# Optimization experiments

Hardware: AMD Instinct MI355X
Metric: run time of the kernel (lower is better)

Reference implementation:

```python
import jax, jax.numpy as jnp
import numpy as np

B, S, L, H = 8, 4, 512, 768
N_SPANS, T_MAX = 4096, 16
N_PAIRS = 16384


def setup_inputs() -> dict:
    key = jax.random.key(0)
    k1, k2, k3, k4, k5, k6 = jax.random.split(key, 6)
    hidden = jax.random.normal(k1, (B, S, L, H), dtype=jnp.float32)
    span_doc = jax.random.randint(k2, (N_SPANS,), 0, B, dtype=jnp.int32)
    # per-span padded, sorted subtoken indices into the flattened S*L window axis
    span_tok = jnp.sort(jax.random.randint(k3, (N_SPANS, T_MAX), 0, S * L, dtype=jnp.int32), axis=1)
    span_len = jax.random.randint(k4, (N_SPANS,), 1, T_MAX + 1, dtype=jnp.int32)
    pair_i = jax.random.randint(k5, (N_PAIRS,), 0, N_SPANS, dtype=jnp.int32)
    pair_j = jax.random.randint(k6, (N_PAIRS,), 0, N_SPANS, dtype=jnp.int32)
    return {"hidden": hidden, "span_doc": span_doc, "span_tok": span_tok,
            "span_len": span_len, "pair_i": pair_i, "pair_j": pair_j}


def reference(hidden, span_doc, span_tok, span_len, pair_i, pair_j):
    # hidden: [B, S, L, H]; flatten windows so span_tok indexes S*L directly
    b, s, l, h = hidden.shape
    hf = hidden.reshape(b, s * l, h)
    # ragged gather: [N, T, H]
    g = hf[span_doc[:, None], span_tok]
    n, t = span_tok.shape
    mask = (jnp.arange(t, dtype=jnp.int32)[None, :] < span_len[:, None])  # [N, T]
    denom = span_len.astype(hidden.dtype)[:, None]
    mean = jnp.sum(g * mask[..., None].astype(hidden.dtype), axis=1) / denom  # [N, H]
    first = g[:, 0]                                      # first subtoken of span
    last = g[jnp.arange(n), span_len - 1]                # last valid subtoken
    reprs = jnp.concatenate([first, mean, last], axis=-1)  # [N, 3H]
    pairs = jnp.concatenate([reprs[pair_i], reprs[pair_j]], axis=-1)  # [P, 6H]
    return pairs
```

## Files before the change

### kernel.cpp

```cpp
#include <hip/hip_runtime.h>


#define SPAN_HF4  192
#define SPAN_TMAX 16
#define SPAN_SL   2048
#define REPR_F4   576
#define OUT_F4    1152
#define MAX_SPANS 4096

typedef float f4nt __attribute__((ext_vector_type(4)));

__device__ __forceinline__ void nt_store_f4(const float4 v, float4* p) {
    f4nt t;
    t.x = v.x; t.y = v.y; t.z = v.z; t.w = v.w;
    __builtin_nontemporal_store(t, reinterpret_cast<f4nt*>(p));
}

__device__ __forceinline__ void store_repr(float4* o, int c,
                                           const float4 a0, const float4 a1,
                                           const float4 a2) {
    nt_store_f4(a0, &o[c]);
    nt_store_f4(a1, &o[SPAN_HF4 + c]);
    nt_store_f4(a2, &o[2 * SPAN_HF4 + c]);
}


__global__ void zero_counts_kernel(int* __restrict__ counts, int n) {
    const int i = blockIdx.x * blockDim.x + threadIdx.x;
    if (i < n) counts[i] = 0;
}

__global__ void count_uses_kernel(const int* __restrict__ pair_i,
                                  const int* __restrict__ pair_j,
                                  int* __restrict__ counts, int n_pairs) {
    const int p = blockIdx.x * blockDim.x + threadIdx.x;
    if (p < n_pairs) {
        atomicAdd(&counts[pair_i[p]], 1);
        atomicAdd(&counts[pair_j[p]], 1);
    }
}

__global__ __launch_bounds__(1024)
void scan_offsets_kernel(const int* __restrict__ counts,
                         int* __restrict__ offsets,
                         int* __restrict__ cursor,
                         int n_spans) {
    __shared__ int sums[1024];
    const int t = threadIdx.x;
    const int base = t * 4;
    int c0 = 0, c1 = 0, c2 = 0, c3 = 0;
    if (base     < n_spans) c0 = counts[base];
    if (base + 1 < n_spans) c1 = counts[base + 1];
    if (base + 2 < n_spans) c2 = counts[base + 2];
    if (base + 3 < n_spans) c3 = counts[base + 3];
    sums[t] = c0 + c1 + c2 + c3;
    __syncthreads();
    for (int off = 1; off < 1024; off <<= 1) {
        const int v = (t >= off) ? sums[t - off] : 0;
        __syncthreads();
        sums[t] += v;
        __syncthreads();
    }
    const int excl = (t == 0) ? 0 : sums[t - 1];
    const int o0 = excl, o1 = o0 + c0, o2 = o1 + c1, o3 = o2 + c2;
    if (base     < n_spans) { offsets[base]     = o0; cursor[base]     = o0; }
    if (base + 1 < n_spans) { offsets[base + 1] = o1; cursor[base + 1] = o1; }
    if (base + 2 < n_spans) { offsets[base + 2] = o2; cursor[base + 2] = o2; }
    if (base + 3 < n_spans) { offsets[base + 3] = o3; cursor[base + 3] = o3; }
    if (t == 1023) offsets[n_spans] = sums[1023];
}

__global__ void fill_targets_kernel(const int* __restrict__ pair_i,
                                    const int* __restrict__ pair_j,
                                    int* __restrict__ cursor,
                                    int* __restrict__ targets,
                                    int n_pairs) {
    const int p = blockIdx.x * blockDim.x + threadIdx.x;
    if (p < n_pairs) {
        const int a = atomicAdd(&cursor[pair_i[p]], 1);
        targets[a] = p * 2;
        const int b = atomicAdd(&cursor[pair_j[p]], 1);
        targets[b] = p * 2 + 1;
    }
}


__global__ __launch_bounds__(192)
void span_scatter_kernel(
    const float4* __restrict__ hidden,
    const int*    __restrict__ span_doc,
    const int*    __restrict__ span_tok,
    const int*    __restrict__ span_len,
    const int*    __restrict__ offsets,
    const int*    __restrict__ targets,
    float4*       __restrict__ out,
    int n_spans)
{
    const int c = threadIdx.x;
    const int s = blockIdx.x;
    if (s >= n_spans) return;

    const int doc   = __builtin_amdgcn_readfirstlane(span_doc[s]);
    const int len   = __builtin_amdgcn_readfirstlane(span_len[s]);
    const int start = __builtin_amdgcn_readfirstlane(offsets[s]);
    const int end   = __builtin_amdgcn_readfirstlane(offsets[s + 1]);
    const int* toks = span_tok + s * SPAN_TMAX;
    const float4* base = hidden + (size_t)doc * (SPAN_SL * SPAN_HF4);

    float4 first, last;
    float sx, sy, sz, sw;
    {
        const float4 v = base[(size_t)toks[0] * SPAN_HF4 + c];
        first = v; last = v;
        sx = v.x; sy = v.y; sz = v.z; sw = v.w;
    }
    #pragma unroll
    for (int t = 1; t < SPAN_TMAX; ++t) {
        const int tc = (t < len) ? t : (len - 1);
        const float4 v = base[(size_t)toks[tc] * SPAN_HF4 + c];
        last = v;
        const float m = (t < len) ? 1.f : 0.f;
        sx += v.x * m; sy += v.y * m; sz += v.z * m; sw += v.w * m;
    }
    const float inv = 1.0f / (float)len;
    const float4 a1 = make_float4(sx * inv, sy * inv, sz * inv, sw * inv);

    int k = start;
    for (; k + 4 <= end; k += 4) {
        const int t0 = __builtin_amdgcn_readfirstlane(targets[k]);
        const int t1 = __builtin_amdgcn_readfirstlane(targets[k + 1]);
        const int t2 = __builtin_amdgcn_readfirstlane(targets[k + 2]);
        const int t3 = __builtin_amdgcn_readfirstlane(targets[k + 3]);
        store_repr(out + (size_t)(t0 >> 1) * OUT_F4 + (size_t)(t0 & 1) * REPR_F4,
                   c, first, a1, last);
        store_repr(out + (size_t)(t1 >> 1) * OUT_F4 + (size_t)(t1 & 1) * REPR_F4,
                   c, first, a1, last);
        store_repr(out + (size_t)(t2 >> 1) * OUT_F4 + (size_t)(t2 & 1) * REPR_F4,
                   c, first, a1, last);
        store_repr(out + (size_t)(t3 >> 1) * OUT_F4 + (size_t)(t3 & 1) * REPR_F4,
                   c, first, a1, last);
    }
    for (; k < end; ++k) {
        const int tv = __builtin_amdgcn_readfirstlane(targets[k]);
        store_repr(out + (size_t)(tv >> 1) * OUT_F4 + (size_t)(tv & 1) * REPR_F4,
                   c, first, a1, last);
    }
}


__global__ __launch_bounds__(192)
void span_fused_kernel(
    const float4* __restrict__ hidden,
    const int*    __restrict__ span_doc,
    const int*    __restrict__ span_tok,
    const int*    __restrict__ span_len,
    const int*    __restrict__ pair_i,
    const int*    __restrict__ pair_j,
    float4*       __restrict__ out)
{
    const int p = blockIdx.x;
    const int c = threadIdx.x;
    const int si = pair_i[p];
    const int sj = pair_j[p];
    float4* orow = out + (size_t)p * OUT_F4;

    #pragma unroll
    for (int side = 0; side < 2; ++side) {
        const int s   = side ? sj : si;
        const int doc = span_doc[s];
        const int len = span_len[s];
        const int* toks = span_tok + s * SPAN_TMAX;
        const float4* base = hidden + (size_t)doc * (SPAN_SL * SPAN_HF4);

        float4 first = make_float4(0.f, 0.f, 0.f, 0.f);
        float4 last  = make_float4(0.f, 0.f, 0.f, 0.f);
        float sx = 0.f, sy = 0.f, sz = 0.f, sw = 0.f;
        #pragma unroll
        for (int t = 0; t < SPAN_TMAX; ++t) {
            const int tc = (t < len) ? t : (len - 1);
            const float4 v = base[(size_t)toks[tc] * SPAN_HF4 + c];
            if (t == 0) first = v;
            last = v;
            const float m = (t < len) ? 1.f : 0.f;
            sx += v.x * m; sy += v.y * m; sz += v.z * m; sw += v.w * m;
        }
        const float inv = 1.0f / (float)len;
        float4* o = orow + side * REPR_F4;
        nt_store_f4(first, &o[c]);
        nt_store_f4(make_float4(sx * inv, sy * inv, sz * inv, sw * inv),
                    &o[SPAN_HF4 + c]);
        nt_store_f4(last, &o[2 * SPAN_HF4 + c]);
    }
}


extern "C" void kernel_launch(void* const* d_in, const int* in_sizes, int n_in,
                              void* d_out, int out_size, void* d_ws, size_t ws_size,
                              hipStream_t stream) {
    const float4* hidden  = (const float4*)d_in[0];
    const int* span_doc   = (const int*)d_in[1];
    const int* span_tok   = (const int*)d_in[2];
    const int* span_len   = (const int*)d_in[3];
    const int* pair_i     = (const int*)d_in[4];
    const int* pair_j     = (const int*)d_in[5];
    float4* out           = (float4*)d_out;

    const int n_spans = in_sizes[1];
    const int n_pairs = in_sizes[4];

    auto align16 = [](size_t x) { return (x + 15) & ~(size_t)15; };
    const size_t counts_b  = align16((size_t)n_spans * sizeof(int));
    const size_t offsets_b = align16((size_t)(n_spans + 1) * sizeof(int));
    const size_t cursor_b  = align16((size_t)n_spans * sizeof(int));
    const size_t targets_b = align16((size_t)2 * n_pairs * sizeof(int));
    const size_t need = counts_b + offsets_b + cursor_b + targets_b;

    if (n_spans <= MAX_SPANS && ws_size >= need) {
        char* ws = (char*)d_ws;
        int* counts  = (int*)(ws);
        int* offsets = (int*)(ws + counts_b);
        int* cursor  = (int*)(ws + counts_b + offsets_b);
        int* targets = (int*)(ws + counts_b + offsets_b + cursor_b);

        const int zb = (n_spans + 255) / 256;
        const int pb = (n_pairs + 255) / 256;
        zero_counts_kernel<<<zb, 256, 0, stream>>>(counts, n_spans);
        count_uses_kernel<<<pb, 256, 0, stream>>>(pair_i, pair_j, counts, n_pairs);
        scan_offsets_kernel<<<1, 1024, 0, stream>>>(counts, offsets, cursor, n_spans);
        fill_targets_kernel<<<pb, 256, 0, stream>>>(pair_i, pair_j, cursor, targets, n_pairs);
        span_scatter_kernel<<<n_spans, 192, 0, stream>>>(
            hidden, span_doc, span_tok, span_len, offsets, targets, out, n_spans);
    } else {
        span_fused_kernel<<<n_pairs, 192, 0, stream>>>(
            hidden, span_doc, span_tok, span_len, pair_i, pair_j, out);
    }
}
```

Baseline: 363.9 us.

## Fuse index-building kernels into one single-block kernel using LDS atomics

Replaces the four preprocessing kernels (zero counts, count uses, scan offsets, fill targets) with one 1024-thread block that counts in shared memory, scans, and fills targets using shared-memory atomic cursors. This removes three kernel launches and the global atomics and buffers for counts and cursors. The cost is that the counting and filling work, previously spread across many blocks, now runs on a single CU.

```diff
diff --git a/kernel.cpp b/kernel.cpp
--- a/kernel.cpp
+++ b/kernel.cpp
@@ -25,34 +25,32 @@
 }
 
 
-__global__ void zero_counts_kernel(int* __restrict__ counts, int n) {
-    const int i = blockIdx.x * blockDim.x + threadIdx.x;
-    if (i < n) counts[i] = 0;
-}
-
-__global__ void count_uses_kernel(const int* __restrict__ pair_i,
-                                  const int* __restrict__ pair_j,
-                                  int* __restrict__ counts, int n_pairs) {
-    const int p = blockIdx.x * blockDim.x + threadIdx.x;
-    if (p < n_pairs) {
-        atomicAdd(&counts[pair_i[p]], 1);
-        atomicAdd(&counts[pair_j[p]], 1);
-    }
-}
-
 __global__ __launch_bounds__(1024)
-void scan_offsets_kernel(const int* __restrict__ counts,
-                         int* __restrict__ offsets,
-                         int* __restrict__ cursor,
-                         int n_spans) {
+void build_index_kernel(const int* __restrict__ pair_i,
+                        const int* __restrict__ pair_j, int n_pairs,
+                        int* __restrict__ offsets,
+                        int* __restrict__ targets,
+                        int n_spans)
+{
+    __shared__ int cnt[MAX_SPANS];
     __shared__ int sums[1024];
     const int t = threadIdx.x;
+
+    for (int i = t; i < n_spans; i += 1024) cnt[i] = 0;
+    __syncthreads();
+
+    for (int p = t; p < n_pairs; p += 1024) {
+        atomicAdd(&cnt[pair_i[p]], 1);
+        atomicAdd(&cnt[pair_j[p]], 1);
+    }
+    __syncthreads();
+
     const int base = t * 4;
     int c0 = 0, c1 = 0, c2 = 0, c3 = 0;
-    if (base     < n_spans) c0 = counts[base];
-    if (base + 1 < n_spans) c1 = counts[base + 1];
-    if (base + 2 < n_spans) c2 = counts[base + 2];
-    if (base + 3 < n_spans) c3 = counts[base + 3];
+    if (base     < n_spans) c0 = cnt[base];
+    if (base + 1 < n_spans) c1 = cnt[base + 1];
+    if (base + 2 < n_spans) c2 = cnt[base + 2];
+    if (base + 3 < n_spans) c3 = cnt[base + 3];
     sums[t] = c0 + c1 + c2 + c3;
     __syncthreads();
     for (int off = 1; off < 1024; off <<= 1) {
@@ -63,23 +61,18 @@
     }
     const int excl = (t == 0) ? 0 : sums[t - 1];
     const int o0 = excl, o1 = o0 + c0, o2 = o1 + c1, o3 = o2 + c2;
-    if (base     < n_spans) { offsets[base]     = o0; cursor[base]     = o0; }
-    if (base + 1 < n_spans) { offsets[base + 1] = o1; cursor[base + 1] = o1; }
-    if (base + 2 < n_spans) { offsets[base + 2] = o2; cursor[base + 2] = o2; }
-    if (base + 3 < n_spans) { offsets[base + 3] = o3; cursor[base + 3] = o3; }
+    __syncthreads();
+    if (base     < n_spans) { offsets[base]     = o0; cnt[base]     = o0; }
+    if (base + 1 < n_spans) { offsets[base + 1] = o1; cnt[base + 1] = o1; }
+    if (base + 2 < n_spans) { offsets[base + 2] = o2; cnt[base + 2] = o2; }
+    if (base + 3 < n_spans) { offsets[base + 3] = o3; cnt[base + 3] = o3; }
     if (t == 1023) offsets[n_spans] = sums[1023];
-}
-
-__global__ void fill_targets_kernel(const int* __restrict__ pair_i,
-                                    const int* __restrict__ pair_j,
-                                    int* __restrict__ cursor,
-                                    int* __restrict__ targets,
-                                    int n_pairs) {
-    const int p = blockIdx.x * blockDim.x + threadIdx.x;
-    if (p < n_pairs) {
-        const int a = atomicAdd(&cursor[pair_i[p]], 1);
+    __syncthreads();
+
+    for (int p = t; p < n_pairs; p += 1024) {
+        const int a = atomicAdd(&cnt[pair_i[p]], 1);
         targets[a] = p * 2;
-        const int b = atomicAdd(&cursor[pair_j[p]], 1);
+        const int b = atomicAdd(&cnt[pair_j[p]], 1);
         targets[b] = p * 2 + 1;
     }
 }
@@ -209,25 +202,17 @@
     const int n_pairs = in_sizes[4];
 
     auto align16 = [](size_t x) { return (x + 15) & ~(size_t)15; };
-    const size_t counts_b  = align16((size_t)n_spans * sizeof(int));
     const size_t offsets_b = align16((size_t)(n_spans + 1) * sizeof(int));
-    const size_t cursor_b  = align16((size_t)n_spans * sizeof(int));
     const size_t targets_b = align16((size_t)2 * n_pairs * sizeof(int));
-    const size_t need = counts_b + offsets_b + cursor_b + targets_b;
+    const size_t need = offsets_b + targets_b;
 
     if (n_spans <= MAX_SPANS && ws_size >= need) {
         char* ws = (char*)d_ws;
-        int* counts  = (int*)(ws);
-        int* offsets = (int*)(ws + counts_b);
-        int* cursor  = (int*)(ws + counts_b + offsets_b);
-        int* targets = (int*)(ws + counts_b + offsets_b + cursor_b);
-
-        const int zb = (n_spans + 255) / 256;
-        const int pb = (n_pairs + 255) / 256;
-        zero_counts_kernel<<<zb, 256, 0, stream>>>(counts, n_spans);
-        count_uses_kernel<<<pb, 256, 0, stream>>>(pair_i, pair_j, counts, n_pairs);
-        scan_offsets_kernel<<<1, 1024, 0, stream>>>(counts, offsets, cursor, n_spans);
-        fill_targets_kernel<<<pb, 256, 0, stream>>>(pair_i, pair_j, cursor, targets, n_pairs);
+        int* offsets = (int*)(ws);
+        int* targets = (int*)(ws + offsets_b);
+
+        build_index_kernel<<<1, 1024, 0, stream>>>(
+            pair_i, pair_j, n_pairs, offsets, targets, n_spans);
         span_scatter_kernel<<<n_spans, 192, 0, stream>>>(
             hidden, span_doc, span_tok, span_len, offsets, targets, out, n_spans);
     } else {
```

New measurement: 381.3 us. 4.8% more time.
